# Kernel optimization log

Measured on AMD Instinct MI355X. Metric: run time of the kernel, lower is better.

## Reference

```python
import jax, jax.numpy as jnp
import numpy as np
import math

N, C, V, T = 64, 192, 25, 300
D = 192  # dim2

def setup_inputs() -> dict:
    key = jax.random.key(0)
    k0, k1, k2, k3 = jax.random.split(key, 4)
    x1 = jax.random.normal(k0, (N, C, V, T), dtype=jnp.float32)
    w1 = jax.random.normal(k1, (D, C), dtype=jnp.float32) * 0.05
    w2 = jax.random.normal(k2, (D, C), dtype=jnp.float32) * 0.05
    w_mask = jax.random.normal(k3, (1, C), dtype=jnp.float32) * 0.05
    return {"x1": x1, "w1": w1, "w2": w2, "w_mask": w_mask}

def reference(x1, w1, w2, w_mask):
    # 1x1 conv projections: contract over channel dim C -> D, layout [N,T,D,V]
    g1 = jnp.einsum('ncvt,dc->ntdv', x1, w1)
    g2 = jnp.einsum('ncvt,dc->ntdv', x1, w2)
    # mean-center over the joint axis V (matches g.mean(2) on [B, D, V])
    g1 = g1 - g1.mean(axis=-1, keepdims=True)
    g2 = g2 - g2.mean(axis=-1, keepdims=True)
    scale = math.sqrt(D)
    # sim_map[n,t,v,w] = sum_d g1[n,t,d,v] * g2[n,t,d,w]
    sim = jnp.einsum('ntdv,ntdw->ntvw', g1, g2) / scale
    # mask: 1x1 conv to 1 channel -> [N,T,V], broadcast over rows (added along last dim)
    mask = jnp.einsum('ncvt,c->ntv', x1, w_mask[0])  # [N,T,V]
    logits = sim + mask[:, :, None, :]
    out = jax.nn.softmax(logits, axis=-1)  # [N, T, V, V]
    return out
```

## Files before the change

kernel.cpp:

```cpp
#include <hip/hip_runtime.h>
#include <hip/hip_bf16.h>
#include <cstdint>
#include <cstddef>

#define NN 64
#define CC 192
#define VV 25
#define TTT 300
#define TC 16
#define NTC 19
#define GRID (NN*NTC)

#define MFRAG_OFF 40960
#define WML_OFF 77824

#define ROWT 88
#define TILE_B 35840
#define MLDS_OFF 71680
#define WMLDS_OFF 145408
#define LDS_TOTAL 145792
#define MCPY_CHUNKS 4632

typedef unsigned short u16;
typedef unsigned long long u64;
typedef short bf16x8 __attribute__((ext_vector_type(8)));
typedef float f32x4 __attribute__((ext_vector_type(4)));
typedef float f4 __attribute__((ext_vector_type(4)));
typedef int i32x4 __attribute__((ext_vector_type(4)));

__device__ __forceinline__ u16 f2bf(float x) {
  union { float f; uint32_t u; } v; v.f = x;
  uint32_t r = v.u + 0x7fffu + ((v.u >> 16) & 1u);
  return (u16)(r >> 16);
}
__device__ __forceinline__ u64 pack4(f32x4 a) {
  return (u64)f2bf(a[0]) | ((u64)f2bf(a[1]) << 16) |
         ((u64)f2bf(a[2]) << 32) | ((u64)f2bf(a[3]) << 48);
}

__global__ __launch_bounds__(192) void prep(const float* __restrict__ w1,
                                            const float* __restrict__ w2,
                                            const float* __restrict__ wm,
                                            u16* __restrict__ mb) {
  int c2 = threadIdx.x, b = blockIdx.x;
  if (b < CC) {
    float s = 0.f;
    for (int d = 0; d < CC; ++d) s += w1[d * CC + b] * w2[d * CC + c2];
    u16 h = f2bf(s);
    int cc = b >> 5, half = (b >> 4) & 1, lr = b & 15;
    int ks = c2 >> 5, l8 = (c2 & 31) >> 3, e = c2 & 7;
    int lane = l8 * 16 + lr;
    mb[MFRAG_OFF + (((cc * 2 + half) * 6 + ks) * 64 + lane) * 8 + e] = h;
  } else {
    mb[WML_OFF + c2] = f2bf(wm[c2]);
  }
}

__device__ __forceinline__ void ldround(const float* __restrict__ xb, int ct,
                                        int tid, bool lastch, f4 pf[4]) {
  #pragma unroll
  for (int it = 0; it < 4; ++it) {
    int job = it * 1024 + tid;
    if (job < 3200) {
      int seg = job & 3;
      int r = job >> 2;
      int v = r >> 5, cl = r & 31;
      int sege = (lastch && seg == 3) ? 2 : seg;
      pf[it] = *(const f4*)(xb + (size_t)(ct * 32 + cl) * (VV * TTT) + v * TTT + sege * 4);
    }
  }
}

__global__ __launch_bounds__(1024, 4) void fused(const float* __restrict__ x1,
                                                 const u16* __restrict__ mb,
                                                 float* __restrict__ out) {
  extern __shared__ char lds[];
  const int tid = threadIdx.x;
  const int wid = tid >> 6, lane = tid & 63, lr = lane & 15, lq = lane >> 4;
  char* YS = lds + wid * 3072;

  {
    const char* src = (const char*)mb + (size_t)MFRAG_OFF * 2;
    #pragma unroll
    for (int k = 0; k < 5; ++k) {
      int i = k * 1024 + tid;
      if (i < MCPY_CHUNKS)
        *(i32x4*)(lds + MLDS_OFF + i * 16) = *(const i32x4*)(src + i * 16);
    }
  }

  int b = blockIdx.x;
  int logical = (b & 7) * (GRID / 8) + (b >> 3);
  int n = logical / NTC;
  int ch = logical - n * NTC;
  int t0 = ch * TC;
  int t = t0 + wid;
  const bool lastch = (t0 + TC > TTT);

  const float* xb = x1 + (size_t)n * (CC * VV * TTT) + t0;

  bf16x8 sf[2][6];
  f4 pf[4];
  ldround(xb, 0, tid, lastch, pf);
  #pragma unroll
  for (int ct = 0; ct < 6; ++ct) {
    f4 cur[4];
    #pragma unroll
    for (int i = 0; i < 4; ++i) cur[i] = pf[i];
    if (ct < 5) ldround(xb, ct + 1, tid, lastch, pf);

    char* buf = lds + (ct & 1) * TILE_B;
    #pragma unroll
    for (int it = 0; it < 4; ++it) {
      int job = it * 1024 + tid;
      if (job < 3200) {
        int seg = job & 3;
        int r = job >> 2;
        int v = r >> 5, cl = r & 31;
        f4 a = cur[it];
        char* base = buf + (size_t)(seg * 100 + v) * ROWT + cl * 2;
        *(u16*)(base)             = f2bf(a[0]);
        *(u16*)(base + 25 * ROWT) = f2bf(a[1]);
        *(u16*)(base + 50 * ROWT) = f2bf(a[2]);
        *(u16*)(base + 75 * ROWT) = f2bf(a[3]);
      }
    }
    __syncthreads();
    #pragma unroll
    for (int j = 0; j < 2; ++j)
      sf[j][ct] = *(const bf16x8*)(buf + (wid * VV + j * 16 + lr) * ROWT + lq * 16);
  }
  __syncthreads();

  f32x4 pacc[2][2], macc[2];
  #pragma unroll
  for (int i = 0; i < 2; ++i) {
    macc[i] = (f32x4){0.f, 0.f, 0.f, 0.f};
    #pragma unroll
    for (int jx = 0; jx < 2; ++jx) pacc[i][jx] = (f32x4){0.f, 0.f, 0.f, 0.f};
  }

  const char* mfl = lds + MLDS_OFF;
  #pragma unroll
  for (int cc = 0; cc < 6; ++cc) {
    f32x4 y00 = (f32x4){0.f,0.f,0.f,0.f}, y01 = y00, y10 = y00, y11 = y00;
    #pragma unroll
    for (int ks = 0; ks < 6; ++ks) {
      bf16x8 a0 = *(const bf16x8*)(mfl + (size_t)((cc * 12 + ks) * 64 + lane) * 16);
      bf16x8 a1 = *(const bf16x8*)(mfl + (size_t)((cc * 12 + 6 + ks) * 64 + lane) * 16);
      y00 = __builtin_amdgcn_mfma_f32_16x16x32_bf16(a0, sf[0][ks], y00, 0, 0, 0);
      y01 = __builtin_amdgcn_mfma_f32_16x16x32_bf16(a1, sf[0][ks], y01, 0, 0, 0);
      y10 = __builtin_amdgcn_mfma_f32_16x16x32_bf16(a0, sf[1][ks], y10, 0, 0, 0);
      y11 = __builtin_amdgcn_mfma_f32_16x16x32_bf16(a1, sf[1][ks], y11, 0, 0, 0);
    }
    *(u64*)(YS + (lr) * 80 + lq * 8) = pack4(y00);
    *(u64*)(YS + (lr) * 80 + 32 + lq * 8) = pack4(y01);
    *(u64*)(YS + (16 + lr) * 80 + lq * 8) = pack4(y10);
    *(u64*)(YS + (16 + lr) * 80 + 32 + lq * 8) = pack4(y11);

    bf16x8 wmf = *(const bf16x8*)(lds + WMLDS_OFF + (cc * 32 + lq * 8) * 2);
    macc[0] = __builtin_amdgcn_mfma_f32_16x16x32_bf16(sf[0][cc], wmf, macc[0], 0, 0, 0);
    macc[1] = __builtin_amdgcn_mfma_f32_16x16x32_bf16(sf[1][cc], wmf, macc[1], 0, 0, 0);

    bf16x8 B0 = *(const bf16x8*)(YS + (lr) * 80 + lq * 16);
    bf16x8 B1 = *(const bf16x8*)(YS + (16 + lr) * 80 + lq * 16);
    pacc[0][0] = __builtin_amdgcn_mfma_f32_16x16x32_bf16(sf[0][cc], B0, pacc[0][0], 0, 0, 0);
    pacc[0][1] = __builtin_amdgcn_mfma_f32_16x16x32_bf16(sf[0][cc], B1, pacc[0][1], 0, 0, 0);
    pacc[1][0] = __builtin_amdgcn_mfma_f32_16x16x32_bf16(sf[1][cc], B0, pacc[1][0], 0, 0, 0);
    pacc[1][1] = __builtin_amdgcn_mfma_f32_16x16x32_bf16(sf[1][cc], B1, pacc[1][1], 0, 0, 0);
  }

  float* SIMW = (float*)YS;
  #pragma unroll
  for (int vt = 0; vt < 2; ++vt)
    #pragma unroll
    for (int wt = 0; wt < 2; ++wt) {
      int w = wt * 16 + lr;
      if (w < VV) {
        #pragma unroll
        for (int i = 0; i < 4; ++i) {
          int v = vt * 16 + lq * 4 + i;
          if (v < VV) SIMW[v * 28 + w] = pacc[vt][wt][i];
        }
      }
    }
  if (lr == 0) {
    #pragma unroll
    for (int j = 0; j < 2; ++j)
      #pragma unroll
      for (int i = 0; i < 4; ++i) {
        int v = j * 16 + lq * 4 + i;
        if (v < VV) SIMW[26 * 28 + v] = macc[j][i];
      }
  }

  f32x4 r[6];
  float r24 = 0.f, rs = 0.f, cs = 0.f;
  if (lane < VV) {
    const f32x4* rp = (const f32x4*)(SIMW + lane * 28);
    #pragma unroll
    for (int k = 0; k < 6; ++k) r[k] = rp[k];
    r24 = SIMW[lane * 28 + 24];
    f32x4 s4 = r[0] + r[1] + r[2] + r[3] + r[4] + r[5];
    rs = s4[0] + s4[1] + s4[2] + s4[3] + r24;
    #pragma unroll
    for (int v = 0; v < VV; ++v) cs += SIMW[v * 28 + lane];
    SIMW[25 * 28 + lane] = cs;
  }
  float x = (lane < VV) ? cs : 0.f;
  #pragma unroll
  for (int s = 1; s < 64; s <<= 1) x += __shfl_xor(x, s);
  const float tot = x;

  if (lane < VV) {
    const int v = lane;
    const float base = -rs * 0.04f + tot * 0.0016f;
    const float isc = 0.07216878364870323f;
    const f32x4* cp = (const f32x4*)(SIMW + 25 * 28);
    const f32x4* mp = (const f32x4*)(SIMW + 26 * 28);
    float l[VV];
    float mx = -1e30f;
    #pragma unroll
    for (int k = 0; k < 6; ++k) {
      f32x4 val = (r[k] - cp[k] * 0.04f + base) * isc + mp[k];
      #pragma unroll
      for (int j = 0; j < 4; ++j) {
        l[k * 4 + j] = val[j];
        mx = fmaxf(mx, val[j]);
      }
    }
    {
      float val = (r24 - SIMW[25 * 28 + 24] * 0.04f + base) * isc + SIMW[26 * 28 + 24];
      l[24] = val;
      mx = fmaxf(mx, val);
    }
    float sum = 0.f;
    #pragma unroll
    for (int w = 0; w < VV; ++w) { float e = __expf(l[w] - mx); l[w] = e; sum += e; }
    float rsc = 1.0f / sum;
    f32x4* wp = (f32x4*)(SIMW + v * 28);
    #pragma unroll
    for (int k = 0; k < 6; ++k) {
      f32x4 o = (f32x4){l[k*4] * rsc, l[k*4+1] * rsc, l[k*4+2] * rsc, l[k*4+3] * rsc};
      wp[k] = o;
    }
    SIMW[v * 28 + 24] = l[24] * rsc;
  }

  if (t < TTT) {
    float* ob = out + (size_t)(n * TTT + t) * 625;
    int v = (lane * 1311) >> 15;
    int w = lane - v * 25;
    #pragma unroll
    for (int i = 0; i < 10; ++i) {
      int idx = lane + i * 64;
      if (idx < 625) ob[idx] = SIMW[v * 28 + w];
      w += 14; v += 2;
      if (w >= 25) { w -= 25; ++v; }
    }
  }
}

extern "C" void kernel_launch(void* const* d_in, const int* in_sizes, int n_in,
                              void* d_out, int out_size, void* d_ws, size_t ws_size,
                              hipStream_t stream) {
  const float* x1 = (const float*)d_in[0];
  const float* w1 = (const float*)d_in[1];
  const float* w2 = (const float*)d_in[2];
  const float* wm = (const float*)d_in[3];
  float* out = (float*)d_out;
  u16* mb = (u16*)d_ws;

  hipLaunchKernelGGL(prep, dim3(CC + 1), dim3(CC), 0, stream, w1, w2, wm, mb);
  hipLaunchKernelGGL(fused, dim3(GRID), dim3(1024), LDS_TOTAL, stream, x1, mb, out);
}
```

Baseline: 172.6 us.

## Stream x tiles directly to LDS with global_load_lds in finer double-buffered stages

Replaces the register-staged load of x (4 float4 per thread per 32-channel round, 6 rounds) with direct global-to-LDS async loads (global_load_lds) in 24 rounds of 8 channels each, with double-buffered raw and bf16 tiles. Threads then convert raw LDS floats to bf16 tiles, and each lane quarter picks up its fragment slice one round later. This is meant to free registers and overlap global loads with conversion. The cost is four times as many barrier rounds, extra LDS traffic and a larger LDS footprint, which may reduce occupancy.

```diff
diff --git a/kernel.cpp b/kernel.cpp
--- a/kernel.cpp
+++ b/kernel.cpp
@@ -14,11 +14,13 @@
 #define MFRAG_OFF 40960
 #define WML_OFF 77824
 
-#define ROWT 88
-#define TILE_B 35840
-#define MLDS_OFF 71680
-#define WMLDS_OFF 145408
-#define LDS_TOTAL 145792
+#define RAW_STRIDE 13312
+#define TILE_OFF 26624
+#define TILE_STRIDE 6512
+#define YS_OFF 39648
+#define MLDS_OFF 88800
+#define WMLDS_OFF 162528
+#define LDS_TOTAL 162912
 #define MCPY_CHUNKS 4632
 
 typedef unsigned short u16;
@@ -56,28 +58,13 @@
   }
 }
 
-__device__ __forceinline__ void ldround(const float* __restrict__ xb, int ct,
-                                        int tid, bool lastch, f4 pf[4]) {
-  #pragma unroll
-  for (int it = 0; it < 4; ++it) {
-    int job = it * 1024 + tid;
-    if (job < 3200) {
-      int seg = job & 3;
-      int r = job >> 2;
-      int v = r >> 5, cl = r & 31;
-      int sege = (lastch && seg == 3) ? 2 : seg;
-      pf[it] = *(const f4*)(xb + (size_t)(ct * 32 + cl) * (VV * TTT) + v * TTT + sege * 4);
-    }
-  }
-}
-
 __global__ __launch_bounds__(1024, 4) void fused(const float* __restrict__ x1,
                                                  const u16* __restrict__ mb,
                                                  float* __restrict__ out) {
   extern __shared__ char lds[];
   const int tid = threadIdx.x;
   const int wid = tid >> 6, lane = tid & 63, lr = lane & 15, lq = lane >> 4;
-  char* YS = lds + wid * 3072;
+  char* YS = lds + YS_OFF + wid * 3072;
 
   {
     const char* src = (const char*)mb + (size_t)MFRAG_OFF * 2;
@@ -99,38 +86,69 @@
 
   const float* xb = x1 + (size_t)n * (CC * VV * TTT) + t0;
 
+  auto issue = [&](int ct) {
+    if (wid < 13) {
+      int k = wid * 64 + lane;
+      int kk = k > 799 ? 799 : k;
+      int cl = kk / 100;
+      int rem = kk - cl * 100;
+      int v = rem >> 2;
+      int seg = kk & 3;
+      int sege = (lastch && seg == 3) ? 2 : seg;
+      const float* src = xb + (size_t)(ct * 8 + cl) * (VV * TTT) + v * TTT + sege * 4;
+      char* dst = lds + (ct & 1) * RAW_STRIDE + wid * 1024;
+      __builtin_amdgcn_global_load_lds(
+          (const __attribute__((address_space(1))) void*)src,
+          (__attribute__((address_space(3))) void*)dst, 16, 0, 0);
+    }
+  };
+
   bf16x8 sf[2][6];
-  f4 pf[4];
-  ldround(xb, 0, tid, lastch, pf);
-  #pragma unroll
-  for (int ct = 0; ct < 6; ++ct) {
-    f4 cur[4];
-    #pragma unroll
-    for (int i = 0; i < 4; ++i) cur[i] = pf[i];
-    if (ct < 5) ldround(xb, ct + 1, tid, lastch, pf);
-
-    char* buf = lds + (ct & 1) * TILE_B;
-    #pragma unroll
-    for (int it = 0; it < 4; ++it) {
-      int job = it * 1024 + tid;
-      if (job < 3200) {
-        int seg = job & 3;
-        int r = job >> 2;
-        int v = r >> 5, cl = r & 31;
-        f4 a = cur[it];
-        char* base = buf + (size_t)(seg * 100 + v) * ROWT + cl * 2;
-        *(u16*)(base)             = f2bf(a[0]);
-        *(u16*)(base + 25 * ROWT) = f2bf(a[1]);
-        *(u16*)(base + 50 * ROWT) = f2bf(a[2]);
-        *(u16*)(base + 75 * ROWT) = f2bf(a[3]);
-      }
-    }
-    __syncthreads();
-    #pragma unroll
-    for (int j = 0; j < 2; ++j)
-      sf[j][ct] = *(const bf16x8*)(buf + (wid * VV + j * 16 + lr) * ROWT + lq * 16);
+  asm volatile("s_waitcnt vmcnt(0)" ::: "memory");
+  issue(0);
+  for (int ct = 0; ct < 24; ++ct) {
+    __builtin_amdgcn_s_barrier();
+    if (ct < 23) {
+      issue(ct + 1);
+      asm volatile("s_waitcnt vmcnt(1)" ::: "memory");
+    } else {
+      asm volatile("s_waitcnt vmcnt(0)" ::: "memory");
+    }
+    __builtin_amdgcn_s_barrier();
+
+    if (tid < 800) {
+      int cl = tid / 100;
+      int rem = tid - cl * 100;
+      int v = rem >> 2;
+      int seg = tid & 3;
+      f4 a = *(const f4*)(lds + (ct & 1) * RAW_STRIDE + tid * 16);
+      char* tb = lds + TILE_OFF + (ct & 1) * TILE_STRIDE + (size_t)v * 16 + cl * 2;
+      *(u16*)(tb + (size_t)(seg * 4 + 0) * 25 * 16) = f2bf(a[0]);
+      *(u16*)(tb + (size_t)(seg * 4 + 1) * 25 * 16) = f2bf(a[1]);
+      *(u16*)(tb + (size_t)(seg * 4 + 2) * 25 * 16) = f2bf(a[2]);
+      *(u16*)(tb + (size_t)(seg * 4 + 3) * 25 * 16) = f2bf(a[3]);
+    }
+
+    if (ct > 0) {
+      int cp = ct - 1;
+      if (lq == (cp & 3)) {
+        const char* tp = lds + TILE_OFF + (cp & 1) * TILE_STRIDE;
+        bf16x8 f0 = *(const bf16x8*)(tp + (size_t)(wid * VV + lr) * 16);
+        bf16x8 f1 = *(const bf16x8*)(tp + (size_t)(wid * VV + 16 + lr) * 16);
+        sf[0][cp >> 2] = f0;
+        sf[1][cp >> 2] = f1;
+      }
+    }
   }
   __syncthreads();
+  {
+    int cp = 23;
+    if (lq == (cp & 3)) {
+      const char* tp = lds + TILE_OFF + (cp & 1) * TILE_STRIDE;
+      sf[0][cp >> 2] = *(const bf16x8*)(tp + (size_t)(wid * VV + lr) * 16);
+      sf[1][cp >> 2] = *(const bf16x8*)(tp + (size_t)(wid * VV + 16 + lr) * 16);
+    }
+  }
 
   f32x4 pacc[2][2], macc[2];
   #pragma unroll
@@ -216,13 +234,13 @@
     const int v = lane;
     const float base = -rs * 0.04f + tot * 0.0016f;
     const float isc = 0.07216878364870323f;
-    const f32x4* cp = (const f32x4*)(SIMW + 25 * 28);
+    const f32x4* cp4 = (const f32x4*)(SIMW + 25 * 28);
     const f32x4* mp = (const f32x4*)(SIMW + 26 * 28);
     float l[VV];
     float mx = -1e30f;
     #pragma unroll
     for (int k = 0; k < 6; ++k) {
-      f32x4 val = (r[k] - cp[k] * 0.04f + base) * isc + mp[k];
+      f32x4 val = (r[k] - cp4[k] * 0.04f + base) * isc + mp[k];
       #pragma unroll
       for (int j = 0; j < 4; ++j) {
         l[k * 4 + j] = val[j];
```

New measurement: 163.6 us. 5.2% less time.
